# Performance work log

Measured on AMD Instinct MI355X. Metric: run time of the kernel, lower is better.

Reference implementation:

```python
import jax, jax.numpy as jnp
import numpy as np

N = 100000   # nodes
E = 1600000  # edges (avg degree 16)
D = 128      # in = hidden = out channels
N_MID = 4    # middle GCN layers (layer_num=6 -> 1 in + 4 mid + 1 out)
BN_EPS = 1e-5


def setup_inputs() -> dict:
    key = jax.random.key(0)
    ks = jax.random.split(key, 6)
    scale = 1.0 / np.sqrt(D)
    x = jax.random.normal(ks[0], (N, D), dtype=jnp.float32)
    edge_index = jax.random.randint(ks[1], (2, E), 0, N, dtype=jnp.int64)
    W0 = jax.random.normal(ks[2], (D, D), dtype=jnp.float32) * scale
    Wmid = jax.random.normal(ks[3], (N_MID, D, D), dtype=jnp.float32) * scale
    Wlast = jax.random.normal(ks[4], (D, D), dtype=jnp.float32) * scale
    return {
        "x": x,
        "edge_index": edge_index,
        "W0": W0,
        "b0": jnp.zeros((D,), jnp.float32),
        "Wmid": Wmid,
        "bmid": jnp.zeros((N_MID, D), jnp.float32),
        "Wlast": Wlast,
        "blast": jnp.zeros((D,), jnp.float32),
        "gamma": jnp.ones((N_MID + 1, D), jnp.float32),
        "beta": jnp.zeros((N_MID + 1, D), jnp.float32),
    }


def _gcn_layer(x, W, b, src, dst, norm, n):
    # GCNConv: h = x @ W; out[dst] += norm_e * h[src]; + bias
    h = x @ W                         # [N, D_out]
    msg = h[src] * norm[:, None]      # [E+N, D_out] gathered + scaled
    return jax.ops.segment_sum(msg, dst, num_segments=n) + b


def _batchnorm(h, g, b):
    # training-mode BatchNorm1d over nodes (biased variance)
    mu = h.mean(axis=0)
    var = h.var(axis=0)
    return (h - mu) * jax.lax.rsqrt(var + BN_EPS) * g + b


def reference(x, edge_index, W0, b0, Wmid, bmid, Wlast, blast, gamma, beta):
    n = x.shape[0]
    # add self-loops (PyG GCNConv default), symmetric normalization
    loop = jnp.arange(n, dtype=edge_index.dtype)
    src = jnp.concatenate([edge_index[0], loop])
    dst = jnp.concatenate([edge_index[1], loop])
    deg = jax.ops.segment_sum(jnp.ones_like(src, dtype=x.dtype), dst, num_segments=n)
    dinv = jnp.where(deg > 0, deg ** -0.5, 0.0)
    norm = dinv[src] * dinv[dst]      # [E+N]

    # layer 0: no residual; dropout is identity in eval (deterministic reference)
    h = _gcn_layer(x, W0, b0, src, dst, norm, n)
    x = jax.nn.relu(_batchnorm(h, gamma[0], beta[0]))
    # middle layers: residual
    for i in range(N_MID):
        h = _gcn_layer(x, Wmid[i], bmid[i], src, dst, norm, n)
        x = jax.nn.relu(_batchnorm(h, gamma[i + 1], beta[i + 1])) + x
    # output layer: no norm/relu
    return _gcn_layer(x, Wlast, blast, src, dst, norm, n)
```

## Files before the change

### kernel.cpp

```cpp
#include <hip/hip_runtime.h>

#define D 128
#define BN_EPS 1e-5f

typedef _Float16 half8 __attribute__((ext_vector_type(8)));
typedef float f32x4 __attribute__((ext_vector_type(4)));
typedef unsigned short ushort_t;
typedef unsigned long long ull_t;

__device__ __forceinline__ unsigned short f2h(float f) {
  union { _Float16 h; unsigned short u; } c;
  c.h = (_Float16)f;
  return c.u;
}
__device__ __forceinline__ unsigned int packh(float lo, float hi) {
  return (unsigned int)f2h(lo) | ((unsigned int)f2h(hi) << 16);
}
__device__ __forceinline__ float h2f(unsigned int v) {
  union { unsigned short u; _Float16 h; } c;
  c.u = (unsigned short)v;
  return (float)c.h;
}

__global__ void k_detect(const int* __restrict__ ei, int* __restrict__ flag) {
  if (blockIdx.x == 0 && threadIdx.x == 0) {
    int is64 = 1;
    for (int i = 0; i < 16; i++)
      if (ei[2 * i + 1] != 0) is64 = 0;
    *flag = is64;
  }
}
__device__ __forceinline__ int load_src(const int* ei, int e, int i, int is64) {
  return is64 ? ei[2 * i] : ei[i];
}
__device__ __forceinline__ int load_dst(const int* ei, int e, int i, int is64) {
  return is64 ? ei[2 * e + 2 * i] : ei[e + i];
}

__global__ void k_hist(const int* __restrict__ ei, int* __restrict__ cnt,
                       const int* __restrict__ flag, int e) {
  int i = blockIdx.x * blockDim.x + threadIdx.x;
  if (i < e) {
    int d = load_dst(ei, e, i, *flag);
    atomicAdd(&cnt[d], 1);
  }
}

__global__ void k_dinv(const int* __restrict__ cnt, float* __restrict__ dinv, int n) {
  int i = blockIdx.x * blockDim.x + threadIdx.x;
  if (i < n) dinv[i] = rsqrtf((float)(cnt[i] + 1));
}

__global__ void k_ordA(const int* __restrict__ cnt, int* __restrict__ dfill,
                       int* __restrict__ bbase, int n, int nb) {
  __shared__ int h[256];
  int t = threadIdx.x;
  h[t] = 0;
  __syncthreads();
  int i = blockIdx.x * 256 + t;
  if (i < n) {
    int d = cnt[i];
    if (d > 255) d = 255;
    atomicAdd(&h[d], 1);
  }
  __syncthreads();
  int c = h[t];
  if (c) bbase[t * nb + blockIdx.x] = atomicAdd(&dfill[t], c);
}

__global__ void k_degscan(const int* __restrict__ dfill, int* __restrict__ dbase) {
  if (blockIdx.x == 0 && threadIdx.x == 0) {
    int run = 0;
    for (int i = 0; i < 256; i++) {
      int t = dfill[i];
      dbase[i] = run;
      run += t;
    }
  }
}

__global__ void k_ordB(const int* __restrict__ cnt, const int* __restrict__ dbase,
                       const int* __restrict__ bbase, unsigned int* __restrict__ ord,
                       int* __restrict__ rank, int* __restrict__ sdeg, int n,
                       int nb) {
  __shared__ int h[256];
  int t = threadIdx.x;
  h[t] = 0;
  __syncthreads();
  int i = blockIdx.x * 256 + t;
  if (i < n) {
    int dc = cnt[i];
    int d = dc > 255 ? 255 : dc;
    int loc = atomicAdd(&h[d], 1);
    int pos = dbase[d] + bbase[d * nb + blockIdx.x] + loc;
    ord[pos] = (unsigned int)i;
    rank[i] = pos;
    sdeg[pos] = dc + 1;
  }
}

__global__ void k_gscan(const int* __restrict__ sdeg, int* __restrict__ gbase,
                        int ngroups, int n) {
  __shared__ int s[256];
  int t = threadIdx.x;
  int per = (ngroups + 255) / 256;
  int g0 = t * per, g1 = g0 + per;
  if (g1 > ngroups) g1 = ngroups;
  int sum = 0;
  for (int g = g0; g < g1; g++) {
    int m = 0;
    for (int j = 0; j < 16; j++) {
      int idx = g * 16 + j;
      int v = (idx < n) ? sdeg[idx] : 0;
      m = max(m, v);
    }
    int st = (m + 3) & ~3;
    gbase[g] = st;
    sum += st * 16;
  }
  s[t] = sum;
  __syncthreads();
  for (int off = 1; off < 256; off <<= 1) {
    int x = (t >= off) ? s[t - off] : 0;
    __syncthreads();
    s[t] += x;
    __syncthreads();
  }
  int run = s[t] - sum;
  for (int g = g0; g < g1; g++) {
    int st = gbase[g];
    gbase[g] = run;
    run += st * 16;
  }
  if (t == 255) gbase[ngroups] = run;
}

__global__ void k_scatter(const int* __restrict__ ei, const int* __restrict__ rank,
                          const int* __restrict__ gbase, int* __restrict__ fill,
                          const float* __restrict__ dinv, uint2* __restrict__ eh,
                          const int* __restrict__ flag, int e) {
  int i = blockIdx.x * blockDim.x + threadIdx.x;
  if (i < e) {
    int is64 = *flag;
    int s = load_src(ei, e, i, is64);
    int d = load_dst(ei, e, i, is64);
    int slot = atomicAdd(&fill[d], 1);
    int r = rank[d];
    int g = r >> 4, j = r & 15;
    ull_t m = ((ull_t)__float_as_uint(dinv[s] * dinv[d]) << 32) |
              (ull_t)((unsigned int)rank[s] * 32u);
    __builtin_nontemporal_store(m, (ull_t*)&eh[gbase[g] + slot * 16 + j]);
  }
}

__global__ void k_self(const int* __restrict__ cnt, const int* __restrict__ rank,
                       const int* __restrict__ gbase, const float* __restrict__ dinv,
                       uint2* __restrict__ eh, int n, int ntot) {
  int i = blockIdx.x * blockDim.x + threadIdx.x;
  if (i >= ntot) return;
  if (i < n) {
    float di = dinv[i];
    int r = rank[i];
    int g = r >> 4, j = r & 15;
    int gb = gbase[g];
    int stride = (gbase[g + 1] - gb) >> 4;
    ull_t m = ((ull_t)__float_as_uint(di * di) << 32) |
              (ull_t)((unsigned int)r * 32u);
    int c = cnt[i];
    __builtin_nontemporal_store(m, (ull_t*)&eh[gb + c * 16 + j]);
    for (int s = c + 1; s < stride; s++)
      __builtin_nontemporal_store(0ULL, (ull_t*)&eh[gb + s * 16 + j]);
  } else {
    int g = i >> 4, j = i & 15;
    int gb = gbase[g];
    int stride = (gbase[g + 1] - gb) >> 4;
    for (int s = 0; s < stride; s++)
      __builtin_nontemporal_store(0ULL, (ull_t*)&eh[gb + s * 16 + j]);
  }
}

__global__ void k_wconv(const float* __restrict__ W0, const float* __restrict__ Wmid,
                        const float* __restrict__ Wlast, ushort_t* __restrict__ Wf) {
  int i = blockIdx.x * 256 + threadIdx.x;
  if (i >= 6 * 16384) return;
  int l = i >> 14, r = i & 16383;
  int k = r >> 7, c = r & 127;
  const float* W = (l == 0) ? W0 : (l <= 4 ? Wmid + (size_t)(l - 1) * 16384 : Wlast);
  Wf[(size_t)l * 16384 + (((k >> 3) * 128 + c) << 3) + (k & 7)] = f2h(W[r]);
}

__global__ __launch_bounds__(256) void k_gemm(
    const void* __restrict__ src, const ushort_t* __restrict__ Wf,
    ushort_t* __restrict__ Hh, unsigned int* __restrict__ XhNew,
    const unsigned int* __restrict__ XhPrev, const float* __restrict__ stats,
    const float* __restrict__ gamma, const float* __restrict__ beta,
    const unsigned int* __restrict__ ord, int n, int mode) {
  __shared__ ushort_t As[16384];
  __shared__ ushort_t Ws[16384];
  const int t = threadIdx.x;
  const int rowBase = blockIdx.x * 128;
  const int off = t & 15;
  const size_t slice_stride = (size_t)n * 32;

  float sc[8], sh[8];
  if (mode >= 1) {
    float inv_n = 1.0f / (float)n;
#pragma unroll
    for (int j = 0; j < 8; j++) {
      int ch = off * 8 + j;
      float mean = stats[ch] * inv_n;
      float var = stats[128 + ch] * inv_n - mean * mean;
      if (var < 0.f) var = 0.f;
      float is = rsqrtf(var + BN_EPS);
      float s = gamma[ch] * is;
      sc[j] = s;
      sh[j] = beta[ch] - mean * s;
    }
  }

#pragma unroll
  for (int i = 0; i < 8; i++) {
    int c = t + i * 256;
    int row = c >> 4;
    int grow = rowBase + row;
    bool valid = grow < n;
    if (!valid) grow = n - 1;
    unsigned int pk[4];
    if (mode == 0) {
      int orig = (int)ord[grow];
      const float* xp = (const float*)src + (size_t)orig * 128 + off * 8;
      float4 v0 = *(const float4*)xp;
      float4 v1 = *(const float4*)(xp + 4);
      pk[0] = packh(v0.x, v0.y);
      pk[1] = packh(v0.z, v0.w);
      pk[2] = packh(v1.x, v1.y);
      pk[3] = packh(v1.z, v1.w);
    } else {
      const char* ap = (const char*)src + (size_t)(off >> 1) * slice_stride +
                       (size_t)grow * 32 + (off & 1) * 16;
      uint4 av = *(const uint4*)ap;
      float v[8];
      v[0] = h2f(av.x & 0xffff); v[1] = h2f(av.x >> 16);
      v[2] = h2f(av.y & 0xffff); v[3] = h2f(av.y >> 16);
      v[4] = h2f(av.z & 0xffff); v[5] = h2f(av.z >> 16);
      v[6] = h2f(av.w & 0xffff); v[7] = h2f(av.w >> 16);
#pragma unroll
      for (int j = 0; j < 8; j++) v[j] = fmaxf(v[j] * sc[j] + sh[j], 0.f);
      if (mode == 2) {
        uint4 rv = *(const uint4*)(XhPrev + (size_t)grow * 64 + off * 4);
        v[0] += h2f(rv.x & 0xffff); v[1] += h2f(rv.x >> 16);
        v[2] += h2f(rv.y & 0xffff); v[3] += h2f(rv.y >> 16);
        v[4] += h2f(rv.z & 0xffff); v[5] += h2f(rv.z >> 16);
        v[6] += h2f(rv.w & 0xffff); v[7] += h2f(rv.w >> 16);
      }
      pk[0] = packh(v[0], v[1]);
      pk[1] = packh(v[2], v[3]);
      pk[2] = packh(v[4], v[5]);
      pk[3] = packh(v[6], v[7]);
      if (valid) *(uint4*)(XhNew + (size_t)grow * 64 + off * 4) = *(uint4*)pk;
    }
    *(uint4*)(&As[(off * 128 + row) * 8]) = *(uint4*)pk;
  }
#pragma unroll
  for (int i = 0; i < 8; i++) {
    int c = t + i * 256;
    *(uint4*)(&Ws[c * 8]) = *(const uint4*)(Wf + c * 8);
  }
  __syncthreads();

  const int wave = t >> 6, lane = t & 63;
  const int q = lane >> 4, ln = lane & 15;
  const int m0 = wave * 32;

  f32x4 acc[2][8];
#pragma unroll
  for (int mt = 0; mt < 2; mt++)
#pragma unroll
    for (int nt = 0; nt < 8; nt++) acc[mt][nt] = (f32x4){0.f, 0.f, 0.f, 0.f};

#pragma unroll
  for (int kk = 0; kk < 4; kk++) {
    int kg = kk * 4 + q;
    half8 a[2];
#pragma unroll
    for (int mt = 0; mt < 2; mt++)
      a[mt] = *(const half8*)(&As[(kg * 128 + m0 + mt * 16 + ln) * 8]);
    half8 b[8];
#pragma unroll
    for (int nt = 0; nt < 8; nt++)
      b[nt] = *(const half8*)(&Ws[(kg * 128 + nt * 16 + ln) * 8]);
#pragma unroll
    for (int mt = 0; mt < 2; mt++)
#pragma unroll
      for (int nt = 0; nt < 8; nt++)
        acc[mt][nt] =
            __builtin_amdgcn_mfma_f32_16x16x32_f16(a[mt], b[nt], acc[mt][nt], 0, 0, 0);
  }

#pragma unroll
  for (int mt = 0; mt < 2; mt++) {
#pragma unroll
    for (int r = 0; r < 4; r++) {
      int grow = rowBase + m0 + mt * 16 + q * 4 + r;
      if (grow < n) {
#pragma unroll
        for (int nt = 0; nt < 8; nt++) {
          ushort_t* hp = (ushort_t*)((char*)Hh + (size_t)nt * slice_stride +
                                     (size_t)grow * 32);
          hp[ln] = f2h(acc[mt][nt][r]);
        }
      }
    }
  }
}

__global__ __launch_bounds__(256) void k_agg(const char* __restrict__ hb,
                                             const int* __restrict__ gbase,
                                             const uint2* __restrict__ eh,
                                             const unsigned int* __restrict__ ord,
                                             const float* __restrict__ bias,
                                             void* __restrict__ out,
                                             float* __restrict__ stats, int n,
                                             int ngroups, int last) {
  __shared__ float lsum[16], lsq[16];
  const int t = threadIdx.x;
  const int slice = blockIdx.x & 7;
  if (!last) {
    if (t < 16) {
      lsum[t] = 0.f;
      lsq[t] = 0.f;
    }
    __syncthreads();
  }
  const int wave = t >> 6, lane = t & 63;
  const int j = lane >> 2;
  const int c = lane & 3;
  const unsigned int c8 = (unsigned int)c * 8u;
  const size_t plane = (size_t)slice * (size_t)n * 32;
  const char* hbs = hb + plane;
  float4 bv = *(const float4*)(bias + slice * 16 + c * 4);
  float rs0 = 0.f, rs1 = 0.f, rs2 = 0.f, rs3 = 0.f;
  float rq0 = 0.f, rq1 = 0.f, rq2 = 0.f, rq3 = 0.f;

  union HU { uint2 u; _Float16 h[4]; };

  const int nstreams = (gridDim.x >> 3) * 4;
  const int sid = (blockIdx.x >> 3) * 4 + wave;

  for (int gi = sid; gi < ngroups; gi += nstreams) {
    int gb = gbase[gi];
    int dm = (gbase[gi + 1] - gb) >> 4;
    const uint2* mp = eh + gb + j;
    float a0 = 0.f, a1 = 0.f, a2 = 0.f, a3 = 0.f;
    for (int i = 0; i < dm; i += 4) {
      uint2 m0 = mp[(i + 0) * 16];
      uint2 m1 = mp[(i + 1) * 16];
      uint2 m2 = mp[(i + 2) * 16];
      uint2 m3 = mp[(i + 3) * 16];
      HU g0, g1, g2, g3;
      g0.u = *(const uint2*)(hbs + (m0.x + c8));
      g1.u = *(const uint2*)(hbs + (m1.x + c8));
      g2.u = *(const uint2*)(hbs + (m2.x + c8));
      g3.u = *(const uint2*)(hbs + (m3.x + c8));
      float w0 = __uint_as_float(m0.y);
      float w1 = __uint_as_float(m1.y);
      float w2 = __uint_as_float(m2.y);
      float w3 = __uint_as_float(m3.y);
      a0 = fmaf((float)g0.h[0], w0, a0);
      a1 = fmaf((float)g0.h[1], w0, a1);
      a2 = fmaf((float)g0.h[2], w0, a2);
      a3 = fmaf((float)g0.h[3], w0, a3);
      a0 = fmaf((float)g1.h[0], w1, a0);
      a1 = fmaf((float)g1.h[1], w1, a1);
      a2 = fmaf((float)g1.h[2], w1, a2);
      a3 = fmaf((float)g1.h[3], w1, a3);
      a0 = fmaf((float)g2.h[0], w2, a0);
      a1 = fmaf((float)g2.h[1], w2, a1);
      a2 = fmaf((float)g2.h[2], w2, a2);
      a3 = fmaf((float)g2.h[3], w2, a3);
      a0 = fmaf((float)g3.h[0], w3, a0);
      a1 = fmaf((float)g3.h[1], w3, a1);
      a2 = fmaf((float)g3.h[2], w3, a2);
      a3 = fmaf((float)g3.h[3], w3, a3);
    }
    int oi = gi * 16 + j;
    if (oi < n) {
      a0 += bv.x;
      a1 += bv.y;
      a2 += bv.z;
      a3 += bv.w;
      if (last) {
        int nd = (int)ord[oi];
        float4 ov = {a0, a1, a2, a3};
        *(float4*)((float*)out + (size_t)nd * 128 + slice * 16 + c * 4) = ov;
      } else {
        uint2 ov;
        ov.x = packh(a0, a1);
        ov.y = packh(a2, a3);
        char* op = (char*)out + plane + (size_t)oi * 32 + c8;
        __builtin_nontemporal_store(((unsigned long long)ov.y << 32) | ov.x,
                                    (unsigned long long*)op);
        rs0 += a0; rs1 += a1; rs2 += a2; rs3 += a3;
        rq0 += a0 * a0; rq1 += a1 * a1; rq2 += a2 * a2; rq3 += a3 * a3;
      }
    }
  }

  if (!last) {
    rs0 += __shfl_xor(rs0, 4);  rs1 += __shfl_xor(rs1, 4);
    rs2 += __shfl_xor(rs2, 4);  rs3 += __shfl_xor(rs3, 4);
    rq0 += __shfl_xor(rq0, 4);  rq1 += __shfl_xor(rq1, 4);
    rq2 += __shfl_xor(rq2, 4);  rq3 += __shfl_xor(rq3, 4);
    rs0 += __shfl_xor(rs0, 8);  rs1 += __shfl_xor(rs1, 8);
    rs2 += __shfl_xor(rs2, 8);  rs3 += __shfl_xor(rs3, 8);
    rq0 += __shfl_xor(rq0, 8);  rq1 += __shfl_xor(rq1, 8);
    rq2 += __shfl_xor(rq2, 8);  rq3 += __shfl_xor(rq3, 8);
    rs0 += __shfl_xor(rs0, 16); rs1 += __shfl_xor(rs1, 16);
    rs2 += __shfl_xor(rs2, 16); rs3 += __shfl_xor(rs3, 16);
    rq0 += __shfl_xor(rq0, 16); rq1 += __shfl_xor(rq1, 16);
    rq2 += __shfl_xor(rq2, 16); rq3 += __shfl_xor(rq3, 16);
    rs0 += __shfl_xor(rs0, 32); rs1 += __shfl_xor(rs1, 32);
    rs2 += __shfl_xor(rs2, 32); rs3 += __shfl_xor(rs3, 32);
    rq0 += __shfl_xor(rq0, 32); rq1 += __shfl_xor(rq1, 32);
    rq2 += __shfl_xor(rq2, 32); rq3 += __shfl_xor(rq3, 32);
    if (lane < 4) {
      atomicAdd(&lsum[c * 4 + 0], rs0);
      atomicAdd(&lsum[c * 4 + 1], rs1);
      atomicAdd(&lsum[c * 4 + 2], rs2);
      atomicAdd(&lsum[c * 4 + 3], rs3);
      atomicAdd(&lsq[c * 4 + 0], rq0);
      atomicAdd(&lsq[c * 4 + 1], rq1);
      atomicAdd(&lsq[c * 4 + 2], rq2);
      atomicAdd(&lsq[c * 4 + 3], rq3);
    }
    __syncthreads();
    if (t < 16) {
      atomicAdd(&stats[slice * 16 + t], lsum[t]);
      atomicAdd(&stats[128 + slice * 16 + t], lsq[t]);
    }
  }
}

extern "C" void kernel_launch(void* const* d_in, const int* in_sizes, int n_in,
                              void* d_out, int out_size, void* d_ws, size_t ws_size,
                              hipStream_t stream) {
  const float* x_in = (const float*)d_in[0];
  const int* ei = (const int*)d_in[1];
  const float* W0 = (const float*)d_in[2];
  const float* b0 = (const float*)d_in[3];
  const float* Wmid = (const float*)d_in[4];
  const float* bmid = (const float*)d_in[5];
  const float* Wlast = (const float*)d_in[6];
  const float* blast = (const float*)d_in[7];
  const float* gamma = (const float*)d_in[8];
  const float* beta = (const float*)d_in[9];

  const int n = in_sizes[0] / D;
  const int e = in_sizes[1] / 2;
  const int ngroups = (n + 15) / 16;
  const int ntot = ngroups * 16;
  const int nb = (n + 255) / 256;
  const int ec = e + n + 8 * n;

  char* ws = (char*)d_ws;
  size_t off = 0;
  auto alloc = [&](size_t bytes) -> void* {
    void* p = ws + off;
    off += (bytes + 255) & ~(size_t)255;
    return p;
  };
  unsigned int* XhA = (unsigned int*)alloc((size_t)n * 64 * 4);
  unsigned int* XhB = (unsigned int*)alloc((size_t)n * 64 * 4);
  unsigned int* Hh = (unsigned int*)alloc((size_t)n * 64 * 4);
  unsigned int* Ag = (unsigned int*)alloc((size_t)n * 64 * 4);
  ushort_t* Wf = (ushort_t*)alloc((size_t)6 * 16384 * 2);
  float* dinv = (float*)alloc((size_t)n * 4);
  int* flag = (int*)alloc(256);
  unsigned int* ord = (unsigned int*)alloc((size_t)ntot * 4);
  int* rank = (int*)alloc((size_t)n * 4);
  int* gbase = (int*)alloc((size_t)(ngroups + 1) * 4);
  int* dbase = (int*)alloc(256 * 4);
  int* bbase = (int*)alloc((size_t)256 * nb * 4);
  uint2* eh = (uint2*)alloc((size_t)ec * 8);
  int* sdeg = (int*)alloc((size_t)ntot * 4);
  char* zbase = ws + off;
  int* cnt = (int*)alloc((size_t)n * 4);
  int* fill = (int*)alloc((size_t)n * 4);
  int* dfill = (int*)alloc(256 * 4);
  float* stats = (float*)alloc(5 * 256 * 4);
  size_t zbytes = (size_t)((ws + off) - zbase);
  hipMemsetAsync(zbase, 0, zbytes, stream);

  k_detect<<<1, 64, 0, stream>>>(ei, flag);
  int eb = (e + 255) / 256;
  k_hist<<<eb, 256, 0, stream>>>(ei, cnt, flag, e);
  k_dinv<<<nb, 256, 0, stream>>>(cnt, dinv, n);
  k_ordA<<<nb, 256, 0, stream>>>(cnt, dfill, bbase, n, nb);
  k_degscan<<<1, 64, 0, stream>>>(dfill, dbase);
  k_ordB<<<nb, 256, 0, stream>>>(cnt, dbase, bbase, ord, rank, sdeg, n, nb);
  k_gscan<<<1, 256, 0, stream>>>(sdeg, gbase, ngroups, n);
  k_scatter<<<eb, 256, 0, stream>>>(ei, rank, gbase, fill, dinv, eh, flag, e);
  k_self<<<(ntot + 255) / 256, 256, 0, stream>>>(cnt, rank, gbase, dinv, eh, n,
                                                 ntot);
  k_wconv<<<(6 * 16384 + 255) / 256, 256, 0, stream>>>(W0, Wmid, Wlast, Wf);

  const int gemm_blocks = (n + 127) / 128;
  const int agg_blocks = 2048;

  k_gemm<<<gemm_blocks, 256, 0, stream>>>(x_in, Wf, (ushort_t*)Hh, nullptr,
                                          nullptr, nullptr, nullptr, nullptr,
                                          ord, n, 0);
  k_agg<<<agg_blocks, 256, 0, stream>>>((const char*)Hh, gbase, eh, ord, b0, Ag,
                                        stats, n, ngroups, 0);
  unsigned int* xprev = nullptr;
  unsigned int* xnew = XhA;
  for (int L = 1; L <= 4; L++) {
    const float* bL = bmid + (size_t)(L - 1) * D;
    k_gemm<<<gemm_blocks, 256, 0, stream>>>(
        Ag, Wf + (size_t)L * 16384, (ushort_t*)Hh, xnew, xprev,
        stats + (L - 1) * 256, gamma + (L - 1) * D, beta + (L - 1) * D, ord, n,
        (L == 1) ? 1 : 2);
    k_agg<<<agg_blocks, 256, 0, stream>>>((const char*)Hh, gbase, eh, ord, bL,
                                          Ag, stats + L * 256, n, ngroups, 0);
    xprev = xnew;
    xnew = (xnew == XhA) ? XhB : XhA;
  }
  k_gemm<<<gemm_blocks, 256, 0, stream>>>(Ag, Wf + (size_t)5 * 16384,
                                          (ushort_t*)Hh, xnew, xprev,
                                          stats + 4 * 256, gamma + 4 * D,
                                          beta + 4 * D, ord, n, 2);
  k_agg<<<agg_blocks, 256, 0, stream>>>((const char*)Hh, gbase, eh, ord, blast,
                                        d_out, nullptr, n, ngroups, 1);
}
```

Measured before the change: 1.037 ms.

## Pack edge metadata into 32-bit words with fp16 weight and pad groups to 2

Each edge entry shrinks from 8 bytes (fp32 weight plus byte offset) to 4 bytes: the node rank sits in the upper 17 bits and a sign-stripped fp16 normalization weight in the low 15 bits. Per-group degree padding drops from a multiple of 4 to a multiple of 2, and the aggregation loop gains a 2-element tail. The aim is to halve the edge-stream bandwidth in every aggregation pass and cut padded work. The cost is lower precision in the edge weights, a limit of 2^17 on node ranks, and a few extra bit operations per edge.

```diff
diff --git a/kernel.cpp b/kernel.cpp
--- a/kernel.cpp
+++ b/kernel.cpp
@@ -114,7 +114,7 @@
       int v = (idx < n) ? sdeg[idx] : 0;
       m = max(m, v);
     }
-    int st = (m + 3) & ~3;
+    int st = (m + 1) & ~1;
     gbase[g] = st;
     sum += st * 16;
   }
@@ -137,7 +137,8 @@
 
 __global__ void k_scatter(const int* __restrict__ ei, const int* __restrict__ rank,
                           const int* __restrict__ gbase, int* __restrict__ fill,
-                          const float* __restrict__ dinv, uint2* __restrict__ eh,
+                          const float* __restrict__ dinv,
+                          unsigned int* __restrict__ eh,
                           const int* __restrict__ flag, int e) {
   int i = blockIdx.x * blockDim.x + threadIdx.x;
   if (i < e) {
@@ -147,15 +148,15 @@
     int slot = atomicAdd(&fill[d], 1);
     int r = rank[d];
     int g = r >> 4, j = r & 15;
-    ull_t m = ((ull_t)__float_as_uint(dinv[s] * dinv[d]) << 32) |
-              (ull_t)((unsigned int)rank[s] * 32u);
-    __builtin_nontemporal_store(m, (ull_t*)&eh[gbase[g] + slot * 16 + j]);
+    unsigned int m = ((unsigned int)rank[s] << 15) |
+                     (unsigned int)(f2h(dinv[s] * dinv[d]) & 0x7fff);
+    __builtin_nontemporal_store(m, &eh[gbase[g] + slot * 16 + j]);
   }
 }
 
 __global__ void k_self(const int* __restrict__ cnt, const int* __restrict__ rank,
                        const int* __restrict__ gbase, const float* __restrict__ dinv,
-                       uint2* __restrict__ eh, int n, int ntot) {
+                       unsigned int* __restrict__ eh, int n, int ntot) {
   int i = blockIdx.x * blockDim.x + threadIdx.x;
   if (i >= ntot) return;
   if (i < n) {
@@ -164,18 +165,18 @@
     int g = r >> 4, j = r & 15;
     int gb = gbase[g];
     int stride = (gbase[g + 1] - gb) >> 4;
-    ull_t m = ((ull_t)__float_as_uint(di * di) << 32) |
-              (ull_t)((unsigned int)r * 32u);
+    unsigned int m = ((unsigned int)r << 15) |
+                     (unsigned int)(f2h(di * di) & 0x7fff);
     int c = cnt[i];
-    __builtin_nontemporal_store(m, (ull_t*)&eh[gb + c * 16 + j]);
+    __builtin_nontemporal_store(m, &eh[gb + c * 16 + j]);
     for (int s = c + 1; s < stride; s++)
-      __builtin_nontemporal_store(0ULL, (ull_t*)&eh[gb + s * 16 + j]);
+      __builtin_nontemporal_store(0u, &eh[gb + s * 16 + j]);
   } else {
     int g = i >> 4, j = i & 15;
     int gb = gbase[g];
     int stride = (gbase[g + 1] - gb) >> 4;
     for (int s = 0; s < stride; s++)
-      __builtin_nontemporal_store(0ULL, (ull_t*)&eh[gb + s * 16 + j]);
+      __builtin_nontemporal_store(0u, &eh[gb + s * 16 + j]);
   }
 }
 
@@ -316,7 +317,7 @@
 
 __global__ __launch_bounds__(256) void k_agg(const char* __restrict__ hb,
                                              const int* __restrict__ gbase,
-                                             const uint2* __restrict__ eh,
+                                             const unsigned int* __restrict__ eh,
                                              const unsigned int* __restrict__ ord,
                                              const float* __restrict__ bias,
                                              void* __restrict__ out,
@@ -350,22 +351,23 @@
   for (int gi = sid; gi < ngroups; gi += nstreams) {
     int gb = gbase[gi];
     int dm = (gbase[gi + 1] - gb) >> 4;
-    const uint2* mp = eh + gb + j;
+    const unsigned int* mp = eh + gb + j;
     float a0 = 0.f, a1 = 0.f, a2 = 0.f, a3 = 0.f;
-    for (int i = 0; i < dm; i += 4) {
-      uint2 m0 = mp[(i + 0) * 16];
-      uint2 m1 = mp[(i + 1) * 16];
-      uint2 m2 = mp[(i + 2) * 16];
-      uint2 m3 = mp[(i + 3) * 16];
+    int i = 0;
+    for (; i + 4 <= dm; i += 4) {
+      unsigned int m0 = mp[(i + 0) * 16];
+      unsigned int m1 = mp[(i + 1) * 16];
+      unsigned int m2 = mp[(i + 2) * 16];
+      unsigned int m3 = mp[(i + 3) * 16];
       HU g0, g1, g2, g3;
-      g0.u = *(const uint2*)(hbs + (m0.x + c8));
-      g1.u = *(const uint2*)(hbs + (m1.x + c8));
-      g2.u = *(const uint2*)(hbs + (m2.x + c8));
-      g3.u = *(const uint2*)(hbs + (m3.x + c8));
-      float w0 = __uint_as_float(m0.y);
-      float w1 = __uint_as_float(m1.y);
-      float w2 = __uint_as_float(m2.y);
-      float w3 = __uint_as_float(m3.y);
+      g0.u = *(const uint2*)(hbs + (((m0 >> 10) & ~31u) + c8));
+      g1.u = *(const uint2*)(hbs + (((m1 >> 10) & ~31u) + c8));
+      g2.u = *(const uint2*)(hbs + (((m2 >> 10) & ~31u) + c8));
+      g3.u = *(const uint2*)(hbs + (((m3 >> 10) & ~31u) + c8));
+      float w0 = h2f(m0 & 0x7fffu);
+      float w1 = h2f(m1 & 0x7fffu);
+      float w2 = h2f(m2 & 0x7fffu);
+      float w3 = h2f(m3 & 0x7fffu);
       a0 = fmaf((float)g0.h[0], w0, a0);
       a1 = fmaf((float)g0.h[1], w0, a1);
       a2 = fmaf((float)g0.h[2], w0, a2);
@@ -382,6 +384,23 @@
       a1 = fmaf((float)g3.h[1], w3, a1);
       a2 = fmaf((float)g3.h[2], w3, a2);
       a3 = fmaf((float)g3.h[3], w3, a3);
+    }
+    if (i < dm) {
+      unsigned int m0 = mp[(i + 0) * 16];
+      unsigned int m1 = mp[(i + 1) * 16];
+      HU g0, g1;
+      g0.u = *(const uint2*)(hbs + (((m0 >> 10) & ~31u) + c8));
+      g1.u = *(const uint2*)(hbs + (((m1 >> 10) & ~31u) + c8));
+      float w0 = h2f(m0 & 0x7fffu);
+      float w1 = h2f(m1 & 0x7fffu);
+      a0 = fmaf((float)g0.h[0], w0, a0);
+      a1 = fmaf((float)g0.h[1], w0, a1);
+      a2 = fmaf((float)g0.h[2], w0, a2);
+      a3 = fmaf((float)g0.h[3], w0, a3);
+      a0 = fmaf((float)g1.h[0], w1, a0);
+      a1 = fmaf((float)g1.h[1], w1, a1);
+      a2 = fmaf((float)g1.h[2], w1, a2);
+      a3 = fmaf((float)g1.h[3], w1, a3);
     }
     int oi = gi * 16 + j;
     if (oi < n) {
@@ -460,7 +479,7 @@
   const int ngroups = (n + 15) / 16;
   const int ntot = ngroups * 16;
   const int nb = (n + 255) / 256;
-  const int ec = e + n + 8 * n;
+  const int ec = e + 10 * n;
 
   char* ws = (char*)d_ws;
   size_t off = 0;
@@ -481,7 +500,7 @@
   int* gbase = (int*)alloc((size_t)(ngroups + 1) * 4);
   int* dbase = (int*)alloc(256 * 4);
   int* bbase = (int*)alloc((size_t)256 * nb * 4);
-  uint2* eh = (uint2*)alloc((size_t)ec * 8);
+  unsigned int* eh = (unsigned int*)alloc((size_t)ec * 4);
   int* sdeg = (int*)alloc((size_t)ntot * 4);
   char* zbase = ws + off;
   int* cnt = (int*)alloc((size_t)n * 4);
```

Result: faster. 958.3 us (-7.6%).
